# Kernel tuning notes

Hardware: AMD Instinct MI355X
Metric: run time of the kernel (lower is better)

The kernel has to match this reference:

```python
import jax, jax.numpy as jnp
import numpy as np

HEADS = 8
DIM_HEAD = 64
SCALE = DIM_HEAD ** -0.5


def setup_inputs() -> dict:
    key = jax.random.key(0)
    k1, k2, k3 = jax.random.split(key, 3)
    B, N, D = 4, 2048, HEADS * DIM_HEAD  # D = inner_dim = 512
    x = jax.random.normal(k1, (B, N, D), dtype=jnp.float32)
    # nn.Linear weights stored transposed vs torch; here we use [in, out]
    w_qkv = jax.random.normal(k2, (D, 3 * D), dtype=jnp.float32) * (D ** -0.5)
    w_out = jax.random.normal(k3, (D, D), dtype=jnp.float32) * (D ** -0.5)
    b_out = jnp.zeros((D,), dtype=jnp.float32)
    return {"x": x, "w_qkv": w_qkv, "w_out": w_out, "b_out": b_out}


def reference(x, w_qkv, w_out, b_out):
    B, N, D = x.shape
    qkv = x @ w_qkv  # [B, N, 3D]
    q, k, v = jnp.split(qkv, 3, axis=-1)

    def to_heads(t):  # b n (h d) -> b h n d
        return t.reshape(B, N, HEADS, DIM_HEAD).transpose(0, 2, 1, 3)

    q, k, v = to_heads(q), to_heads(k), to_heads(v)
    dots = jnp.einsum('bhnd,bhmd->bhnm', q, k) * SCALE  # [B,H,N,N]
    attn = jax.nn.softmax(dots, axis=-1)
    out = jnp.einsum('bhnm,bhmd->bhnd', attn, v)  # [B,H,N,d]
    out = out.transpose(0, 2, 1, 3).reshape(B, N, D)  # b h n d -> b n (h d)
    return out @ w_out + b_out
```

## Files before the change

kernel.cpp:

```cpp
#include <hip/hip_runtime.h>

typedef __bf16 bf16;
typedef __bf16 bf16x8 __attribute__((ext_vector_type(8)));
typedef __bf16 bf16x4 __attribute__((ext_vector_type(4)));
typedef float f32x4 __attribute__((ext_vector_type(4)));
typedef float f32x16 __attribute__((ext_vector_type(16)));
typedef unsigned int uint2v __attribute__((ext_vector_type(2)));

#define MFMA16(a, b, c) __builtin_amdgcn_mfma_f32_16x16x32_bf16(a, b, c, 0, 0, 0)
#define MFMA32(a, b, c) __builtin_amdgcn_mfma_f32_32x32x16_bf16(a, b, c, 0, 0, 0)

#define CS 0.18033688011112042f

#if __has_builtin(__builtin_amdgcn_exp2f)
#define EXP2(x) __builtin_amdgcn_exp2f(x)
#else
#define EXP2(x) exp2f(x)
#endif

#define WAIT_VM0() __builtin_amdgcn_s_waitcnt(0x0F70)
#define WAIT_VM6() __builtin_amdgcn_s_waitcnt(0x0F76)
#define WAIT_VM8() __builtin_amdgcn_s_waitcnt(0x0F78)

#define BARRIER() __builtin_amdgcn_s_barrier()
#define CFENCE() asm volatile("" ::: "memory")

__device__ __forceinline__ void load_lds16(const bf16* g, bf16* l) {
    __builtin_amdgcn_global_load_lds(
        (const __attribute__((address_space(1))) unsigned int*)g,
        (__attribute__((address_space(3))) unsigned int*)l, 16, 0, 0);
}

#if __has_builtin(__builtin_amdgcn_permlane32_swap)
__device__ __forceinline__ bf16x8 build_bfrag(bf16x4 plo, bf16x4 phi, int ) {
    union { bf16x4 b; unsigned int i[2]; } ul, uh;
    ul.b = plo; uh.b = phi;
    uint2v r0 = __builtin_amdgcn_permlane32_swap(ul.i[0], uh.i[0], false, false);
    uint2v r1 = __builtin_amdgcn_permlane32_swap(ul.i[1], uh.i[1], false, false);
    union { unsigned int i[4]; bf16x8 b; } ub;
    ub.i[0] = r0[0]; ub.i[1] = r1[0]; ub.i[2] = r0[1]; ub.i[3] = r1[1];
    return ub.b;
}

__device__ __forceinline__ float sum_halves(float x) {
    union { float f; unsigned int u; } a; a.f = x;
    uint2v r = __builtin_amdgcn_permlane32_swap(a.u, a.u, false, false);
    union { unsigned int u; float f; } b0, b1;
    b0.u = r[0]; b1.u = r[1];
    return b0.f + b1.f;
}
#else
__device__ __forceinline__ bf16x4 shfl_xor32_b64(bf16x4 v) {
    union { bf16x4 b; int i[2]; } u;
    u.b = v;
    u.i[0] = __shfl_xor(u.i[0], 32, 64);
    u.i[1] = __shfl_xor(u.i[1], 32, 64);
    return u.b;
}
__device__ __forceinline__ bf16x8 build_bfrag(bf16x4 plo, bf16x4 phi, int h) {
    bf16x4 xlo = shfl_xor32_b64(plo);
    bf16x4 xhi = shfl_xor32_b64(phi);
    bf16x4 lo4 = h ? xhi : plo;
    bf16x4 hi4 = h ? phi : xlo;
    bf16x8 bb;
#pragma unroll
    for (int i = 0; i < 4; ++i) { bb[i] = lo4[i]; bb[4 + i] = hi4[i]; }
    return bb;
}
__device__ __forceinline__ float sum_halves(float x) {
    return x + __shfl_xor(x, 32, 64);
}
#endif

__global__ __launch_bounds__(256) void f32_to_bf16_kernel(const float* __restrict__ in,
                                                          bf16* __restrict__ out, int n) {
    int i = (blockIdx.x * 256 + threadIdx.x) * 4;
    if (i < n) {
        float4 v = *(const float4*)&in[i];
        bf16x4 o = {(bf16)v.x, (bf16)v.y, (bf16)v.z, (bf16)v.w};
        *(bf16x4*)&out[i] = o;
    }
}

__global__ __launch_bounds__(256) void transpose_f2b(const float* __restrict__ in,
                                                     bf16* __restrict__ out,
                                                     int R, int C) {
    __shared__ float tile[32][33];
    int tx = threadIdx.x & 31, ty = threadIdx.x >> 5;
    int c0 = blockIdx.x * 32, r0 = blockIdx.y * 32;
#pragma unroll
    for (int i = ty; i < 32; i += 8)
        tile[i][tx] = in[(size_t)(r0 + i) * C + c0 + tx];
    __syncthreads();
#pragma unroll
    for (int i = ty; i < 32; i += 8)
        out[(size_t)(c0 + i) * R + r0 + tx] = (bf16)tile[tx][i];
}

__global__ __launch_bounds__(256) void transpose_v_kernel(const bf16* __restrict__ qkv,
                                                          bf16* __restrict__ vt) {
    __shared__ bf16 tile[32][33];
    int tx = threadIdx.x & 31, ty = threadIdx.x >> 5;
    int bh = blockIdx.z, b = bh >> 3, h = bh & 7;
    int n0 = blockIdx.x * 32, d0 = blockIdx.y * 32;
#pragma unroll
    for (int i = ty; i < 32; i += 8)
        tile[i][tx] = qkv[(size_t)(b * 2048 + n0 + i) * 1536 + 1024 + h * 64 + d0 + tx];
    __syncthreads();
#pragma unroll
    for (int i = ty; i < 32; i += 8)
        vt[(size_t)(bh * 64 + d0 + i) * 2048 + n0 + tx] = tile[tx][i];
}

template <int MT, int MODE, typename OutT>
__global__ __launch_bounds__(256, (MT == 4) ? 2 : 3)
void gemm_bt_kernel(const bf16* __restrict__ A,
                    const bf16* __restrict__ Bt,
                    const float* __restrict__ bias,
                    OutT* __restrict__ C,
                    int M, int N, int K) {
    const int BM = MT * 32;
    const int ASZ = BM * 64, BSZ = 128 * 64;
    __shared__ bf16 As[2 * ASZ];
    __shared__ bf16 Bs[2 * BSZ];
    int t = threadIdx.x;
    int lane = t & 63, w = t >> 6;
    int wr = w >> 1, wc = w & 1;
    int quad = lane >> 4, r16 = lane & 15;

    int lin = blockIdx.y * gridDim.x + blockIdx.x;
    int cpx = (gridDim.x * gridDim.y) >> 3;
    int nl = (lin & 7) * cpx + (lin >> 3);
    int bx = nl % gridDim.x, by = nl / gridDim.x;
    int m0 = by * BM, n0 = bx * 128;

    const f32x4 fzero = {0.f, 0.f, 0.f, 0.f};
    f32x4 acc[MT][4];
#pragma unroll
    for (int i = 0; i < MT; ++i)
#pragma unroll
        for (int j = 0; j < 4; ++j) acc[i][j] = fzero;

    const bf16* ap[MT]; bf16* ad[MT];
    const bf16* bp[4];  bf16* bd[4];
#pragma unroll
    for (int i = 0; i < MT; ++i) {
        int ci = i * 256 + t;
        int row = ci >> 3, cp = ci & 7, cc = cp ^ (row & 7);
        ap[i] = &A[(size_t)(m0 + row) * K + cc * 8];
        ad[i] = &As[ci * 8];
    }
#pragma unroll
    for (int i = 0; i < 4; ++i) {
        int ci = i * 256 + t;
        int row = ci >> 3, cp = ci & 7, cc = cp ^ (row & 7);
        bp[i] = &Bt[(size_t)(n0 + row) * K + cc * 8];
        bd[i] = &Bs[ci * 8];
    }

    auto stage = [&](int par) {
#pragma unroll
        for (int i = 0; i < MT; ++i) { load_lds16(ap[i], ad[i] + par * ASZ); ap[i] += 64; }
#pragma unroll
        for (int i = 0; i < 4; ++i) { load_lds16(bp[i], bd[i] + par * BSZ); bp[i] += 64; }
    };

    stage(0);
    int nk = K >> 6;
    for (int kk = 0; kk < nk; ++kk) {
        if (kk + 1 < nk) {
            stage((kk + 1) & 1);
            if constexpr (MT == 4) WAIT_VM8(); else WAIT_VM6();
        } else {
            WAIT_VM0();
        }
        CFENCE(); BARRIER(); CFENCE();

        const bf16* Asb = &As[(kk & 1) * ASZ];
        const bf16* Bsb = &Bs[(kk & 1) * BSZ];
#pragma unroll
        for (int ks = 0; ks < 2; ++ks) {
            bf16x8 af[MT], bfr[4];
            int cp = (ks * 4 + quad) ^ (r16 & 7);
#pragma unroll
            for (int mt = 0; mt < MT; ++mt)
                af[mt] = *(const bf16x8*)&Asb[(wr * (BM / 2) + mt * 16 + r16) * 64 + cp * 8];
#pragma unroll
            for (int nt = 0; nt < 4; ++nt)
                bfr[nt] = *(const bf16x8*)&Bsb[(wc * 64 + nt * 16 + r16) * 64 + cp * 8];
#pragma unroll
            for (int mt = 0; mt < MT; ++mt)
#pragma unroll
                for (int nt = 0; nt < 4; ++nt)
                    acc[mt][nt] = MFMA16(af[mt], bfr[nt], acc[mt][nt]);
        }
        if (kk + 1 < nk) { CFENCE(); BARRIER(); CFENCE(); }
    }
#pragma unroll
    for (int mt = 0; mt < MT; ++mt)
#pragma unroll
        for (int nt = 0; nt < 4; ++nt)
#pragma unroll
            for (int r = 0; r < 4; ++r) {
                int row = m0 + wr * (BM / 2) + mt * 16 + quad * 4 + r;
                int col = n0 + wc * 64 + nt * 16 + r16;
                float v = acc[mt][nt][r];
                if (MODE == 1 && n0 < 512) v *= CS;
                if (MODE == 2) v += bias[col];
                C[(size_t)row * N + col] = (OutT)v;
            }
}

__global__ __launch_bounds__(128, 2) void attn_kernel(const bf16* __restrict__ qkv,
                                                      const bf16* __restrict__ vt,
                                                      bf16* __restrict__ out) {
    __shared__ __align__(16) char smemraw[32768];
    bf16* stage = (bf16*)smemraw;

    int t = threadIdx.x;
    int lane = t & 63, w = t >> 6;
    int h = lane >> 5, q = lane & 31;

    int lin = blockIdx.y * gridDim.x + blockIdx.x;
    int nl = (lin & 7) * 128 + (lin >> 3);
    int bh = nl >> 5, b = bh >> 3, hd = bh & 7;
    int qb = (nl & 31) * 64;

    bf16x8 qf[2][4];
#pragma unroll
    for (int sub = 0; sub < 2; ++sub) {
        size_t qoff = (size_t)(b * 2048 + qb + sub * 32 + q) * 1536 + hd * 64;
#pragma unroll
        for (int s = 0; s < 4; ++s)
            qf[sub][s] = *(const bf16x8*)&qkv[qoff + s * 16 + h * 8];
    }

    f32x16 o_acc[2][2];
#pragma unroll
    for (int sub = 0; sub < 2; ++sub)
#pragma unroll
        for (int db = 0; db < 2; ++db)
#pragma unroll
            for (int i = 0; i < 16; ++i) o_acc[sub][db][i] = 0.f;
    float psum[2] = {0.f, 0.f};

    bf16* base = stage + w * 8192;

    const bf16* kp[4]; const bf16* vp[4];
    int kdo[4], vdo[4];
#pragma unroll
    for (int rdd = 0; rdd < 4; ++rdd) {
        int ciK = rdd * 64 + lane;
        int rowK = ciK >> 3, ccK = (ciK & 7) ^ (rowK & 7);
        kp[rdd] = &qkv[(size_t)(b * 2048 + w * 1024 + rowK) * 1536 + 512 + hd * 64 + ccK * 8];
        kdo[rdd] = ciK * 8;
        int ciV = rdd * 64 + lane;
        int rowV = ciV >> 2, ccV = (ciV & 3) ^ (rowV & 3);
        vp[rdd] = &vt[(size_t)(bh * 64 + rowV) * 2048 + w * 1024 + ccV * 8];
        vdo[rdd] = 2048 + ciV * 8;
    }

#pragma unroll
    for (int rdd = 0; rdd < 4; ++rdd) {
        load_lds16(kp[rdd], base + kdo[rdd]);  kp[rdd] += (size_t)32 * 1536;
        load_lds16(vp[rdd], base + vdo[rdd]);  vp[rdd] += 32;
    }

    for (int it = 0; it < 32; ++it) {
        const bf16* Ks = base + (it & 1) * 4096;
        const bf16* Vs = Ks + 2048;
        if (it < 31) {
            bf16* nb = base + ((it + 1) & 1) * 4096;
#pragma unroll
            for (int rdd = 0; rdd < 4; ++rdd) {
                load_lds16(kp[rdd], nb + kdo[rdd]);  kp[rdd] += (size_t)32 * 1536;
                load_lds16(vp[rdd], nb + vdo[rdd]);  vp[rdd] += 32;
            }
            WAIT_VM8();
        } else {
            WAIT_VM0();
        }

        bf16x8 kf[4];
#pragma unroll
        for (int s = 0; s < 4; ++s) {
            int cp = (s * 2 + h) ^ (q & 7);
            kf[s] = *(const bf16x8*)&Ks[q * 64 + cp * 8];
        }
        bf16x8 vf[2][2];
#pragma unroll
        for (int kstep = 0; kstep < 2; ++kstep)
#pragma unroll
            for (int db = 0; db < 2; ++db) {
                int cp = (kstep * 2 + h) ^ (q & 3);
                vf[kstep][db] = *(const bf16x8*)&Vs[(db * 32 + q) * 32 + cp * 8];
            }

#pragma unroll
        for (int sub = 0; sub < 2; ++sub) {
            f32x16 sacc;
#pragma unroll
            for (int i = 0; i < 16; ++i) sacc[i] = 0.f;
#pragma unroll
            for (int s = 0; s < 4; ++s)
                sacc = MFMA32(kf[s], qf[sub][s], sacc);

            bf16x4 pk[4];
            float ps0 = 0.f, ps1 = 0.f, ps2 = 0.f, ps3 = 0.f;
#pragma unroll
            for (int i = 0; i < 4; ++i) {
                float p0 = EXP2(sacc[i]);
                float p1 = EXP2(sacc[4 + i]);
                float p2 = EXP2(sacc[8 + i]);
                float p3 = EXP2(sacc[12 + i]);
                ps0 += p0; ps1 += p1; ps2 += p2; ps3 += p3;
                pk[0][i] = (bf16)p0; pk[1][i] = (bf16)p1;
                pk[2][i] = (bf16)p2; pk[3][i] = (bf16)p3;
            }
            psum[sub] += (ps0 + ps1) + (ps2 + ps3);
            bf16x8 bfr0 = build_bfrag(pk[0], pk[1], h);
            bf16x8 bfr1 = build_bfrag(pk[2], pk[3], h);

#pragma unroll
            for (int db = 0; db < 2; ++db) {
                o_acc[sub][db] = MFMA32(vf[0][db], bfr0, o_acc[sub][db]);
                o_acc[sub][db] = MFMA32(vf[1][db], bfr1, o_acc[sub][db]);
            }
        }
    }

    float l_own[2];
#pragma unroll
    for (int sub = 0; sub < 2; ++sub)
        l_own[sub] = sum_halves(psum[sub]);

    __syncthreads();
    float* Of = (float*)smemraw;
    float* Lf = (float*)(smemraw + 17408);

    if (w == 1) {
#pragma unroll
        for (int sub = 0; sub < 2; ++sub) {
#pragma unroll
            for (int db = 0; db < 2; ++db)
#pragma unroll
                for (int r = 0; r < 16; ++r) {
                    int d = db * 32 + (r & 3) + 8 * (r >> 2) + 4 * h;
                    Of[(sub * 32 + q) * 68 + d] = o_acc[sub][db][r];
                }
            if (h == 0) Lf[sub * 32 + q] = l_own[sub];
        }
    }
    __syncthreads();
    if (w == 0) {
#pragma unroll
        for (int sub = 0; sub < 2; ++sub) {
#pragma unroll
            for (int db = 0; db < 2; ++db)
#pragma unroll
                for (int r = 0; r < 16; ++r) {
                    int d = db * 32 + (r & 3) + 8 * (r >> 2) + 4 * h;
                    Of[(sub * 32 + q) * 68 + d] += o_acc[sub][db][r];
                }
            if (h == 0) Lf[sub * 32 + q] += l_own[sub];
        }
    }
    __syncthreads();

    {
        int row = t >> 1, half = t & 1;
        float linv = 1.f / Lf[row];
        const float* src = &Of[row * 68 + half * 32];
        bf16* dst = &out[(size_t)(b * 2048 + qb + row) * 512 + hd * 64 + half * 32];
#pragma unroll
        for (int i = 0; i < 4; ++i) {
            f32x4 a = *(const f32x4*)&src[i * 8];
            f32x4 c = *(const f32x4*)&src[i * 8 + 4];
            bf16x8 o8;
#pragma unroll
            for (int j = 0; j < 4; ++j) {
                o8[j] = (bf16)(a[j] * linv);
                o8[4 + j] = (bf16)(c[j] * linv);
            }
            *(bf16x8*)&dst[i * 8] = o8;
        }
    }
}

extern "C" void kernel_launch(void* const* d_in, const int* in_sizes, int n_in,
                              void* d_out, int out_size, void* d_ws, size_t ws_size,
                              hipStream_t stream) {
    const float* x     = (const float*)d_in[0];
    const float* w_qkv = (const float*)d_in[1];
    const float* w_out = (const float*)d_in[2];
    const float* b_out = (const float*)d_in[3];
    float* out = (float*)d_out;

    char* ws = (char*)d_ws;
    size_t off = 0;
    bf16* xb    = (bf16*)(ws + off); off += (size_t)8192 * 512 * 2;
    bf16* wqkvT = (bf16*)(ws + off); off += (size_t)1536 * 512 * 2;
    bf16* woutT = (bf16*)(ws + off); off += (size_t)512 * 512 * 2;
    bf16* qkv   = (bf16*)(ws + off); off += (size_t)8192 * 1536 * 2;
    bf16* vt    = (bf16*)(ws + off); off += (size_t)32 * 64 * 2048 * 2;
    bf16* attn  = (bf16*)(ws + off);

    f32_to_bf16_kernel<<<4096, 256, 0, stream>>>(x, xb, 8192 * 512);
    transpose_f2b<<<dim3(48, 16), 256, 0, stream>>>(w_qkv, wqkvT, 512, 1536);
    transpose_f2b<<<dim3(16, 16), 256, 0, stream>>>(w_out, woutT, 512, 512);
    gemm_bt_kernel<4, 1, bf16><<<dim3(12, 64), 256, 0, stream>>>(
        xb, wqkvT, nullptr, qkv, 8192, 1536, 512);
    transpose_v_kernel<<<dim3(64, 2, 32), 256, 0, stream>>>(qkv, vt);
    attn_kernel<<<dim3(32, 32), 128, 0, stream>>>(qkv, vt, attn);
    gemm_bt_kernel<2, 2, float><<<dim3(4, 128), 256, 0, stream>>>(
        attn, woutT, b_out, out, 8192, 512, 512);
}
```

Before: 167.1 us.

## Fuse input prep kernels, vectorize V transpose, simplify attention block mapping

```diff
diff --git a/kernel.cpp b/kernel.cpp
--- a/kernel.cpp
+++ b/kernel.cpp
@@ -72,22 +72,27 @@
 }
 #endif
 
-__global__ __launch_bounds__(256) void f32_to_bf16_kernel(const float* __restrict__ in,
-                                                          bf16* __restrict__ out, int n) {
-    int i = (blockIdx.x * 256 + threadIdx.x) * 4;
-    if (i < n) {
-        float4 v = *(const float4*)&in[i];
+__global__ __launch_bounds__(256) void prep_kernel(const float* __restrict__ x,
+                                                   const float* __restrict__ w_qkv,
+                                                   const float* __restrict__ w_out,
+                                                   bf16* __restrict__ xb,
+                                                   bf16* __restrict__ wqkvT,
+                                                   bf16* __restrict__ woutT) {
+    __shared__ float tile[32][33];
+    int bid = blockIdx.x, t = threadIdx.x;
+    if (bid < 4096) {
+        int i = (bid * 256 + t) * 4;
+        float4 v = *(const float4*)&x[i];
         bf16x4 o = {(bf16)v.x, (bf16)v.y, (bf16)v.z, (bf16)v.w};
-        *(bf16x4*)&out[i] = o;
-    }
-}
-
-__global__ __launch_bounds__(256) void transpose_f2b(const float* __restrict__ in,
-                                                     bf16* __restrict__ out,
-                                                     int R, int C) {
-    __shared__ float tile[32][33];
-    int tx = threadIdx.x & 31, ty = threadIdx.x >> 5;
-    int c0 = blockIdx.x * 32, r0 = blockIdx.y * 32;
+        *(bf16x4*)&xb[i] = o;
+        return;
+    }
+    const float* in; bf16* out; int C, bx, by;
+    if (bid < 4864) { int b2 = bid - 4096; in = w_qkv; out = wqkvT; C = 1536; bx = b2 % 48; by = b2 / 48; }
+    else            { int b3 = bid - 4864; in = w_out; out = woutT; C = 512;  bx = b3 & 15; by = b3 >> 4; }
+    const int R = 512;
+    int tx = t & 31, ty = t >> 5;
+    int c0 = bx * 32, r0 = by * 32;
 #pragma unroll
     for (int i = ty; i < 32; i += 8)
         tile[i][tx] = in[(size_t)(r0 + i) * C + c0 + tx];
@@ -99,17 +104,24 @@
 
 __global__ __launch_bounds__(256) void transpose_v_kernel(const bf16* __restrict__ qkv,
                                                           bf16* __restrict__ vt) {
-    __shared__ bf16 tile[32][33];
-    int tx = threadIdx.x & 31, ty = threadIdx.x >> 5;
-    int bh = blockIdx.z, b = bh >> 3, h = bh & 7;
-    int n0 = blockIdx.x * 32, d0 = blockIdx.y * 32;
-#pragma unroll
-    for (int i = ty; i < 32; i += 8)
-        tile[i][tx] = qkv[(size_t)(b * 2048 + n0 + i) * 1536 + 1024 + h * 64 + d0 + tx];
+    __shared__ bf16 tile[64][68];
+    int t = threadIdx.x;
+    int bh = blockIdx.z, b = bh >> 3, hd = bh & 7;
+    int n0 = blockIdx.x * 64;
+    int rr = t >> 4, c4 = (t & 15) * 4;
+#pragma unroll
+    for (int p = 0; p < 4; ++p) {
+        int r = p * 16 + rr;
+        *(bf16x4*)&tile[r][c4] =
+            *(const bf16x4*)&qkv[(size_t)(b * 2048 + n0 + r) * 1536 + 1024 + hd * 64 + c4];
+    }
     __syncthreads();
 #pragma unroll
-    for (int i = ty; i < 32; i += 8)
-        vt[(size_t)(bh * 64 + d0 + i) * 2048 + n0 + tx] = tile[tx][i];
+    for (int p = 0; p < 4; ++p) {
+        int d = p * 16 + rr;
+        bf16x4 o = {tile[c4][d], tile[c4 + 1][d], tile[c4 + 2][d], tile[c4 + 3][d]};
+        *(bf16x4*)&vt[(size_t)(bh * 64 + d) * 2048 + n0 + c4] = o;
+    }
 }
 
 template <int MT, int MODE, typename OutT>
@@ -220,11 +232,8 @@
     int t = threadIdx.x;
     int lane = t & 63, w = t >> 6;
     int h = lane >> 5, q = lane & 31;
-
-    int lin = blockIdx.y * gridDim.x + blockIdx.x;
-    int nl = (lin & 7) * 128 + (lin >> 3);
-    int bh = nl >> 5, b = bh >> 3, hd = bh & 7;
-    int qb = (nl & 31) * 64;
+    int bh = blockIdx.y, b = bh >> 3, hd = bh & 7;
+    int qb = blockIdx.x * 64;
 
     bf16x8 qf[2][4];
 #pragma unroll
@@ -405,12 +414,10 @@
     bf16* vt    = (bf16*)(ws + off); off += (size_t)32 * 64 * 2048 * 2;
     bf16* attn  = (bf16*)(ws + off);
 
-    f32_to_bf16_kernel<<<4096, 256, 0, stream>>>(x, xb, 8192 * 512);
-    transpose_f2b<<<dim3(48, 16), 256, 0, stream>>>(w_qkv, wqkvT, 512, 1536);
-    transpose_f2b<<<dim3(16, 16), 256, 0, stream>>>(w_out, woutT, 512, 512);
+    prep_kernel<<<5120, 256, 0, stream>>>(x, w_qkv, w_out, xb, wqkvT, woutT);
     gemm_bt_kernel<4, 1, bf16><<<dim3(12, 64), 256, 0, stream>>>(
         xb, wqkvT, nullptr, qkv, 8192, 1536, 512);
-    transpose_v_kernel<<<dim3(64, 2, 32), 256, 0, stream>>>(qkv, vt);
+    transpose_v_kernel<<<dim3(32, 1, 32), 256, 0, stream>>>(qkv, vt);
     attn_kernel<<<dim3(32, 32), 128, 0, stream>>>(qkv, vt, attn);
     gemm_bt_kernel<2, 2, float><<<dim3(4, 128), 256, 0, stream>>>(
         attn, woutT, b_out, out, 8192, 512, 512);
```

Result: faster. 159.6 us (-4.5%).
